# Performance work log

Measured on AMD Instinct MI355X. Metric: run time of the kernel, lower is better.

Reference implementation:

```python
import jax, jax.numpy as jnp
import numpy as np

B, S, E, H = 4, 2048, 1024, 16
D = E // H  # head_dim = 64

def setup_inputs() -> dict:
    key = jax.random.key(0)
    ks = jax.random.split(key, 9)
    std = 1.0 / np.sqrt(E)
    return {
        "x":  jax.random.normal(ks[0], (B, S, E), jnp.float32),
        "Wq": jax.random.uniform(ks[1], (E, E), jnp.float32, -std, std),
        "bq": jax.random.uniform(ks[2], (E,),   jnp.float32, -std, std),
        "Wk": jax.random.uniform(ks[3], (E, E), jnp.float32, -std, std),
        "bk": jax.random.uniform(ks[4], (E,),   jnp.float32, -std, std),
        "Wv": jax.random.uniform(ks[5], (E, E), jnp.float32, -std, std),
        "bv": jax.random.uniform(ks[6], (E,),   jnp.float32, -std, std),
        "Wo": jax.random.uniform(ks[7], (E, E), jnp.float32, -std, std),
        "bo": jax.random.uniform(ks[8], (E,),   jnp.float32, -std, std),
    }

def reference(x, Wq, bq, Wk, bk, Wv, bv, Wo, bo):
    b, s, e = x.shape
    # QKV projections (weights stored as [in,out] == torch W.T applied as x @ W)
    q = (x @ Wq + bq).reshape(b, s, H, D).transpose(0, 2, 1, 3)  # [B,H,S,D]
    k = (x @ Wk + bk).reshape(b, s, H, D).transpose(0, 2, 1, 3)
    v = (x @ Wv + bv).reshape(b, s, H, D).transpose(0, 2, 1, 3)
    scores = jnp.einsum('bhqd,bhkd->bhqk', q, k) / jnp.sqrt(jnp.float32(D))
    causal = jnp.triu(jnp.ones((s, s), bool), k=1)  # True above diagonal
    scores = jnp.where(causal, -jnp.inf, scores)
    p = jax.nn.softmax(scores, axis=-1)  # dropout disabled (eval mode)
    out = jnp.einsum('bhqk,bhkd->bhqd', p, v)  # [B,H,S,D]
    out = out.transpose(0, 2, 1, 3).reshape(b, s, e)
    return out @ Wo + bo
```

## Files before the change

kernel.cpp:

```cpp
#include <hip/hip_runtime.h>
#include <math.h>

#define E_DIM 1024
#define B_DIM 4
#define S_DIM 2048
#define H_DIM 16
#define D_HEAD 64
#define M_DIM (B_DIM * S_DIM)
#define LOG2E 1.44269504f

typedef _Float16 half8 __attribute__((ext_vector_type(8)));
typedef _Float16 half4 __attribute__((ext_vector_type(4)));
typedef __fp16  fp16x2 __attribute__((ext_vector_type(2)));
typedef float floatx4 __attribute__((ext_vector_type(4)));
typedef unsigned uint2v __attribute__((ext_vector_type(2)));
#define MFMA_F16(a, b, c) __builtin_amdgcn_mfma_f32_16x16x32_f16(a, b, c, 0, 0, 0)

#if __has_builtin(__builtin_amdgcn_exp2f)
#define EXP2F(x) __builtin_amdgcn_exp2f(x)
#else
#define EXP2F(x) exp2f(x)
#endif

union H4 { fp16x2 h2[2]; half4 h4; };
union H8 { fp16x2 h2[4]; half8 h8; };

#define GLDS16(g, l)                                                          \
    __builtin_amdgcn_global_load_lds(                                         \
        (const __attribute__((address_space(1))) void*)(g),                   \
        (__attribute__((address_space(3))) void*)(l), 16, 0, 0)

__device__ const int SEG_QBLK[40] = {3,4,5,6,7,7,8,8,9,9,10,10,11,11,11,12,12,12,
                                     13,13,13,14,14,14,15,15,15,15,
                                     2,6,10,14, 1,5,9,13, 0,4,8,12};
__device__ const int SEG_SEG[40]  = {0,0,0,0,0,1,0,1,0,1,0,1,0,1,2,0,1,2,
                                     0,1,2,0,1,2,0,1,2,3,
                                     0,1,2,3, 0,1,2,3, 0,1,2,3};
__device__ const int SEG_BASE[16] = {0,1,2,3,4,6,8,10,12,15,18,21,24,28,32,36};

__global__ __launch_bounds__(256) void cvt_x(
    const float* __restrict__ X, _Float16* __restrict__ Xh)
{
    size_t i = ((size_t)blockIdx.x * 256 + threadIdx.x) * 8;
    float4 a = *(const float4*)&X[i];
    float4 b = *(const float4*)&X[i + 4];
    half8 h = {(_Float16)a.x, (_Float16)a.y, (_Float16)a.z, (_Float16)a.w,
               (_Float16)b.x, (_Float16)b.y, (_Float16)b.z, (_Float16)b.w};
    *(half8*)&Xh[i] = h;
}

__global__ __launch_bounds__(256) void cvt_w(
    const float* __restrict__ W0, const float* __restrict__ W1,
    const float* __restrict__ W2, const float* __restrict__ W3,
    _Float16* __restrict__ T0, _Float16* __restrict__ T1,
    _Float16* __restrict__ T2, _Float16* __restrict__ T3)
{
    const int z = blockIdx.z;
    const float* W = (z == 0) ? W0 : (z == 1) ? W1 : (z == 2) ? W2 : W3;
    _Float16*   T  = (z == 0) ? T0 : (z == 1) ? T1 : (z == 2) ? T2 : T3;
    const int k0 = blockIdx.x * 64, n0 = blockIdx.y * 64;
    const int tid = threadIdx.x;
    __shared__ float t[64][65];
#pragma unroll
    for (int it = 0; it < 4; it++) {
        int r = it * 16 + (tid >> 4);
        int c = (tid & 15) * 4;
        float4 v = *(const float4*)&W[(size_t)(k0 + r) * E_DIM + n0 + c];
        t[r][c] = v.x; t[r][c + 1] = v.y; t[r][c + 2] = v.z; t[r][c + 3] = v.w;
    }
    __syncthreads();
#pragma unroll
    for (int it = 0; it < 2; it++) {
        int n = it * 32 + (tid >> 3);
        int kk = (tid & 7) * 8;
        half8 h;
#pragma unroll
        for (int j = 0; j < 8; j++) h[j] = (_Float16)t[kk + j][n];
        *(half8*)&T[(size_t)(n0 + n) * E_DIM + k0 + kk] = h;
    }
}

#define STAGE128(t, s)                                                        \
    _Pragma("unroll") for (int i = 0; i < 4; i++) {                           \
        GLDS16(aS[i] + (t) * 64, As + (s) * 8192 + dOff[i]);                  \
        GLDS16(bS[i] + (t) * 64, Bs + (s) * 8192 + dOff[i]);                  \
    }

#define PH128_READ_A(mh)                                                      \
    _Pragma("unroll") for (int am = 0; am < 2; am++)                          \
        _Pragma("unroll") for (int kh = 0; kh < 2; kh++)                      \
            a_[am][kh] = *(const half8*)&As[sb +                              \
                (wr * 64 + ((mh) * 2 + am) * 16 + m16) * 64 +                 \
                (((kh * 4 + quad) ^ sw8) * 8)];

#define PH128_READ_B(nh)                                                      \
    _Pragma("unroll") for (int bn = 0; bn < 2; bn++)                          \
        _Pragma("unroll") for (int kh = 0; kh < 2; kh++)                      \
            b_[bn][kh] = *(const half8*)&Bs[sb +                              \
                (wc * 64 + ((nh) * 2 + bn) * 16 + m16) * 64 +                 \
                (((kh * 4 + quad) ^ sw8) * 8)];

#define PH128_MFMA(mh, nh)                                                    \
    __builtin_amdgcn_s_setprio(1);                                            \
    _Pragma("unroll") for (int am = 0; am < 2; am++)                          \
        _Pragma("unroll") for (int bn = 0; bn < 2; bn++)                      \
            acc[(mh) * 2 + am][(nh) * 2 + bn] =                               \
                MFMA_F16(a_[am][1], b_[bn][1],                                \
                    MFMA_F16(a_[am][0], b_[bn][0],                            \
                             acc[(mh) * 2 + am][(nh) * 2 + bn]));             \
    __builtin_amdgcn_s_setprio(0);

#define GEMM128_CORE(Aptr, Bptr)                                              \
    const int tid = threadIdx.x;                                              \
    const int wave = tid >> 6, lane = tid & 63;                               \
    const int m16 = lane & 15, quad = lane >> 4;                              \
    const int wr = wave >> 1, wc = wave & 1;                                  \
    const int m0 = blockIdx.x * 128, n0 = blockIdx.y * 128;                   \
    const int sw8 = m16 & 7;                                                  \
    __shared__ _Float16 As[2 * 8192];                                         \
    __shared__ _Float16 Bs[2 * 8192];                                         \
    floatx4 acc[4][4];                                                        \
    const floatx4 zf = {0.f, 0.f, 0.f, 0.f};                                  \
    _Pragma("unroll") for (int i = 0; i < 4; i++)                             \
        _Pragma("unroll") for (int j = 0; j < 4; j++) acc[i][j] = zf;         \
    const _Float16* aS[4];                                                    \
    const _Float16* bS[4];                                                    \
    int dOff[4];                                                              \
    _Pragma("unroll") for (int i = 0; i < 4; i++) {                           \
        int u = i * 256 + tid;                                                \
        int ru = u >> 3, cb = (u & 7) ^ (ru & 7);                             \
        aS[i] = (Aptr) + (size_t)(m0 + ru) * E_DIM + cb * 8;                  \
        bS[i] = (Bptr) + (size_t)(n0 + ru) * E_DIM + cb * 8;                  \
        dOff[i] = i * 2048 + wave * 512;                                      \
    }                                                                         \
    STAGE128(0, 0);                                                           \
    STAGE128(1, 1);                                                           \
    asm volatile("s_waitcnt vmcnt(8)" ::: "memory");                          \
    __builtin_amdgcn_s_barrier();                                             \
    half8 a_[2][2], b_[2][2];                                                 \
    for (int t = 0; t < 16; t++) {                                            \
        const int sb = (t & 1) * 8192;                                        \
        PH128_READ_A(0); PH128_READ_B(0); PH128_MFMA(0, 0);                   \
        PH128_READ_B(1); PH128_MFMA(0, 1);                                    \
        PH128_READ_A(1); PH128_MFMA(1, 1);                                    \
        PH128_READ_B(0); PH128_MFMA(1, 0);                                    \
        if (t + 1 < 16) {                                                     \
            asm volatile("s_waitcnt lgkmcnt(0)" ::: "memory");                \
            __builtin_amdgcn_s_barrier();                                     \
            if (t + 2 < 16) {                                                 \
                STAGE128(t + 2, t & 1);                                       \
                asm volatile("s_waitcnt vmcnt(8)" ::: "memory");              \
            } else {                                                          \
                asm volatile("s_waitcnt vmcnt(0)" ::: "memory");              \
            }                                                                 \
            __builtin_amdgcn_s_barrier();                                     \
        }                                                                     \
    }

__global__ __launch_bounds__(256) void qkv_mfma(
    const _Float16* __restrict__ Xh,
    const _Float16* __restrict__ Tq, const float* __restrict__ bq,
    const _Float16* __restrict__ Tk, const float* __restrict__ bk,
    const _Float16* __restrict__ Tv, const float* __restrict__ bv,
    _Float16* __restrict__ Qo, _Float16* __restrict__ Ko, _Float16* __restrict__ Vo)
{
    const int z = blockIdx.z;
    const _Float16* Wt   = (z == 0) ? Tq : (z == 1) ? Tk : Tv;
    const float*    bias = (z == 0) ? bq : (z == 1) ? bk : bv;

    GEMM128_CORE(Xh, Wt)

    if (z == 2) {
#pragma unroll
        for (int nt = 0; nt < 4; nt++) {
            int n = n0 + wc * 64 + nt * 16 + m16;
            int h = n >> 6, d = n & 63;
            int dt = d >> 4, ld = d & 15;
            float bias_v = bias[n];
#pragma unroll
            for (int mt = 0; mt < 4; mt++) {
                int m_b = m0 + wr * 64 + mt * 16 + quad * 4;
                int b = m_b >> 11, s = m_b & 2047;
                int bh = b * H_DIM + h;
                int c = s >> 6, kl = s & 63;
                int kh = kl >> 5, q8 = (kl >> 2) & 3, j0 = ((kl >> 4) & 1) * 4;
                size_t off = ((size_t)bh * 32 + c) * 4096
                           + (size_t)(((dt * 2 + kh) * 64 + q8 * 16 + ld) * 8 + j0);
                half4 hv;
#pragma unroll
                for (int r = 0; r < 4; r++) hv[r] = (_Float16)(acc[mt][nt][r] + bias_v);
                *(half4*)&Vo[off] = hv;
            }
        }
    } else {
        _Float16* Out = (z == 0) ? Qo : Ko;
        const float sc = (z == 0) ? 0.125f * LOG2E : 1.0f;
#pragma unroll
        for (int nt = 0; nt < 4; nt++) {
            int n = n0 + wc * 64 + nt * 16 + m16;
            int h = n >> 6, d = n & 63;
            int dh = d >> 5, qd = (d >> 3) & 3, j = d & 7;
            float bias_v = bias[n];
#pragma unroll
            for (int mt = 0; mt < 4; mt++) {
#pragma unroll
                for (int r = 0; r < 4; r++) {
                    int m = m0 + wr * 64 + mt * 16 + quad * 4 + r;
                    int b = m >> 11, s = m & 2047;
                    int bh = b * H_DIM + h;
                    size_t off;
                    if (z == 0) {
                        int qblk = s >> 7, qq = s & 127;
                        int sub = qq >> 4, lq = qq & 15;
                        off = ((size_t)bh * 16 + qblk) * 8192
                            + (size_t)(((sub * 2 + dh) * 64 + qd * 16 + lq) * 8 + j);
                    } else {
                        int c = s >> 6, kl = s & 63;
                        int kt = kl >> 4, lk = kl & 15;
                        off = ((size_t)bh * 32 + c) * 4096
                            + (size_t)(((kt * 2 + dh) * 64 + qd * 16 + lk) * 8 + j);
                    }
                    Out[off] = (_Float16)((acc[mt][nt][r] + bias_v) * sc);
                }
            }
        }
    }
}

__global__ __launch_bounds__(256) void out_mfma(
    const _Float16* __restrict__ Oh, const _Float16* __restrict__ To,
    const float* __restrict__ bias, float* __restrict__ Out)
{
    GEMM128_CORE(Oh, To)

#pragma unroll
    for (int nt = 0; nt < 4; nt++) {
        int n = n0 + wc * 64 + nt * 16 + m16;
        float bias_v = bias[n];
#pragma unroll
        for (int mt = 0; mt < 4; mt++) {
#pragma unroll
            for (int r = 0; r < 4; r++) {
                int m = m0 + wr * 64 + mt * 16 + quad * 4 + r;
                Out[(size_t)m * E_DIM + n] = acc[mt][nt][r] + bias_v;
            }
        }
    }
}

__global__ __launch_bounds__(256) void attn_mfma(
    const _Float16* __restrict__ Qb, const _Float16* __restrict__ Kb,
    const _Float16* __restrict__ Vb, _Float16* __restrict__ Opart,
    float* __restrict__ Mv, float* __restrict__ Lv, _Float16* __restrict__ O)
{
    const int L = blockIdx.x;
    const int xcd = L & 7;
    const int u = L >> 3;
    const int bh = xcd * 8 + (u / 40);
    const int wid = u % 40;
    const int wave = threadIdx.x >> 6;
    const int qblk = SEG_QBLK[wid];
    const int seg  = SEG_SEG[wid];
    const int q0 = qblk * 128;
    const int c0 = seg * 8;
    const int c1 = min(c0 + 8, 2 * qblk + 2);
    const bool solo = (c0 == 0) && (c1 == 2 * qblk + 2);
    const int lane = threadIdx.x & 63;
    const int m16 = lane & 15, quad = lane >> 4;

    const int qmin = q0 + wave * 32;
    const int qmax = qmin + 31;
    const int c1w = min(c1, (qmax >> 6) + 1);

    const _Float16* gQ = Qb + ((size_t)bh * 16 + qblk) * 8192 + wave * 2048 + lane * 8;
    half8 qf[2][2];
#pragma unroll
    for (int mt = 0; mt < 2; mt++)
#pragma unroll
        for (int dh = 0; dh < 2; dh++)
            qf[mt][dh] = *(const half8*)&gQ[(mt * 2 + dh) * 512];

    const floatx4 zf  = {0.f, 0.f, 0.f, 0.f};
    const floatx4 cm4 = {-4.f, -4.f, -4.f, -4.f};
    half8 onev;
#pragma unroll
    for (int j = 0; j < 8; j++) onev[j] = (_Float16)1.0f;

    floatx4 acco[2][4];
    floatx4 lacc[2];
#pragma unroll
    for (int mt = 0; mt < 2; mt++) {
        lacc[mt] = zf;
#pragma unroll
        for (int dt = 0; dt < 4; dt++) acco[mt][dt] = zf;
    }

    const _Float16* gK = Kb + ((size_t)bh * 32 + c0) * 4096 + lane * 8;
    const _Float16* gV = Vb + ((size_t)bh * 32 + c0) * 4096 + lane * 8;

    half8 kf[4][2];
#pragma unroll
    for (int kt = 0; kt < 4; kt++)
#pragma unroll
        for (int dh = 0; dh < 2; dh++)
            kf[kt][dh] = *(const half8*)&gK[(kt * 2 + dh) * 512];
    gK += 4096;

    for (int c = c0; c < c1w; c++) {
        const int k0 = c * 64;

        half8 vf[4][2];
#pragma unroll
        for (int dt = 0; dt < 4; dt++)
#pragma unroll
            for (int kh = 0; kh < 2; kh++)
                vf[dt][kh] = *(const half8*)&gV[(dt * 2 + kh) * 512];
        gV += 4096;

        floatx4 sf[2][4];
        __builtin_amdgcn_s_setprio(1);
#pragma unroll
        for (int kt = 0; kt < 4; kt++)
#pragma unroll
            for (int mt = 0; mt < 2; mt++)
                sf[mt][kt] = MFMA_F16(kf[kt][1], qf[mt][1],
                               MFMA_F16(kf[kt][0], qf[mt][0], cm4));
        __builtin_amdgcn_s_setprio(0);

        if (c + 1 < c1w) {
#pragma unroll
            for (int kt = 0; kt < 4; kt++)
#pragma unroll
                for (int dh = 0; dh < 2; dh++)
                    kf[kt][dh] = *(const half8*)&gK[(kt * 2 + dh) * 512];
            gK += 4096;
        }

        const bool full = (k0 + 63 <= qmin);
#pragma unroll
        for (int mt = 0; mt < 2; mt++) {
            const int qg = qmin + mt * 16 + m16;
#pragma unroll
            for (int kt = 0; kt < 4; kt++)
#pragma unroll
                for (int r = 0; r < 4; r++) {
                    if (!full) {
                        int key = k0 + kt * 16 + quad * 4 + r;
                        if (key > qg) sf[mt][kt][r] = -INFINITY;
                    }
                }

            H8 u8[2];
#pragma unroll
            for (int kt = 0; kt < 4; kt++) {
                float e0 = EXP2F(sf[mt][kt][0]);
                float e1 = EXP2F(sf[mt][kt][1]);
                float e2 = EXP2F(sf[mt][kt][2]);
                float e3 = EXP2F(sf[mt][kt][3]);
                u8[kt >> 1].h2[(kt & 1) * 2]     = __builtin_amdgcn_cvt_pkrtz(e0, e1);
                u8[kt >> 1].h2[(kt & 1) * 2 + 1] = __builtin_amdgcn_cvt_pkrtz(e2, e3);
            }

            __builtin_amdgcn_s_setprio(1);
            lacc[mt] = MFMA_F16(onev, u8[1].h8,
                         MFMA_F16(onev, u8[0].h8, lacc[mt]));
#pragma unroll
            for (int dt = 0; dt < 4; dt++)
                acco[mt][dt] = MFMA_F16(vf[dt][1], u8[1].h8,
                                 MFMA_F16(vf[dt][0], u8[0].h8, acco[mt][dt]));
            __builtin_amdgcn_s_setprio(0);
        }
    }

    if (solo) {
        const int b = bh >> 4;
        const int h = bh & (H_DIM - 1);
#pragma unroll
        for (int mt = 0; mt < 2; mt++) {
            float inv = 1.f / lacc[mt][0];
            int q = qmin + mt * 16 + m16;
            _Float16* dst = O + (size_t)(b * S_DIM + q) * E_DIM + h * 64;
#pragma unroll
            for (int dt = 0; dt < 4; dt++) {
                H4 u4;
                u4.h2[0] = __builtin_amdgcn_cvt_pkrtz(acco[mt][dt][0] * inv, acco[mt][dt][1] * inv);
                u4.h2[1] = __builtin_amdgcn_cvt_pkrtz(acco[mt][dt][2] * inv, acco[mt][dt][3] * inv);
                *(half4*)&dst[dt * 16 + quad * 4] = u4.h4;
            }
        }
    } else {
        const size_t prow = ((size_t)bh * 40 + SEG_BASE[qblk] + seg) * 128;
#pragma unroll
        for (int mt = 0; mt < 2; mt++) {
            int lq = wave * 32 + mt * 16 + m16;
            if (quad == 0) {
                Lv[prow + lq] = lacc[mt][0];
            }
            _Float16* dst = Opart + (prow + lq) * 64;
#pragma unroll
            for (int dt = 0; dt < 4; dt++) {
                H4 u4;
                u4.h2[0] = __builtin_amdgcn_cvt_pkrtz(acco[mt][dt][0], acco[mt][dt][1]);
                u4.h2[1] = __builtin_amdgcn_cvt_pkrtz(acco[mt][dt][2], acco[mt][dt][3]);
                *(half4*)&dst[dt * 16 + quad * 4] = u4.h4;
            }
        }
    }
}

__global__ __launch_bounds__(256) void attn_combine(
    const _Float16* __restrict__ Opart, const float* __restrict__ Mv,
    const float* __restrict__ Lv, _Float16* __restrict__ O)
{
    const int qb = blockIdx.x + 4, bh = blockIdx.y;
    const int nseg = (qb >> 2) + 1;
    const size_t pbase = ((size_t)bh * 40 + SEG_BASE[qb]) * 128;
    const int t = threadIdx.x;
    const int r = t >> 1, dh = (t & 1) * 32;

    float L = 0.f;
    for (int s = 0; s < nseg; s++) L += Lv[pbase + s * 128 + r];
    const float invL = 1.f / L;

    const int b = bh >> 4, h = bh & (H_DIM - 1);
    const int q = qb * 128 + r;
    _Float16* dst = O + (size_t)(b * S_DIM + q) * E_DIM + h * 64 + dh;
#pragma unroll
    for (int d0 = 0; d0 < 32; d0 += 8) {
        float acc[8] = {0.f, 0.f, 0.f, 0.f, 0.f, 0.f, 0.f, 0.f};
        for (int s = 0; s < nseg; s++) {
            half8 v = *(const half8*)&Opart[(pbase + s * 128 + r) * 64 + dh + d0];
#pragma unroll
            for (int j = 0; j < 8; j++) acc[j] += (float)v[j];
        }
        half8 o;
#pragma unroll
        for (int j = 0; j < 8; j++) o[j] = (_Float16)(acc[j] * invL);
        *(half8*)&dst[d0] = o;
    }
}

extern "C" void kernel_launch(void* const* d_in, const int* in_sizes, int n_in,
                              void* d_out, int out_size, void* d_ws, size_t ws_size,
                              hipStream_t stream) {
    const float* x  = (const float*)d_in[0];
    const float* Wq = (const float*)d_in[1];
    const float* bq = (const float*)d_in[2];
    const float* Wk = (const float*)d_in[3];
    const float* bk = (const float*)d_in[4];
    const float* Wv = (const float*)d_in[5];
    const float* bv = (const float*)d_in[6];
    const float* Wo = (const float*)d_in[7];
    const float* bo = (const float*)d_in[8];

    const size_t SZ = (size_t)M_DIM * E_DIM;
    const size_t WZ = (size_t)E_DIM * E_DIM;
    _Float16* Xh = (_Float16*)d_ws;
    _Float16* Tq = Xh + SZ;
    _Float16* Tk = Tq + WZ;
    _Float16* Tv = Tk + WZ;
    _Float16* To = Tv + WZ;
    _Float16* Qb = To + WZ;
    _Float16* Kb = Qb + SZ;
    _Float16* Vb = Kb + SZ;
    _Float16* Opart = Vb + SZ;
    float* Mv = (float*)(Opart + (size_t)2560 * 8192);
    float* Lv = Mv + 2560 * 128;
    _Float16* Oh = Xh;

    cvt_x<<<dim3(M_DIM * E_DIM / 2048), 256, 0, stream>>>(x, Xh);
    cvt_w<<<dim3(16, 16, 4), 256, 0, stream>>>(Wq, Wk, Wv, Wo, Tq, Tk, Tv, To);

    qkv_mfma<<<dim3(M_DIM / 128, E_DIM / 128, 3), 256, 0, stream>>>(
        Xh, Tq, bq, Tk, bk, Tv, bv, Qb, Kb, Vb);

    attn_mfma<<<dim3(8 * 8 * 40), 256, 0, stream>>>(
        Qb, Kb, Vb, Opart, Mv, Lv, Oh);

    attn_combine<<<dim3(12, B_DIM * H_DIM), 256, 0, stream>>>(Opart, Mv, Lv, Oh);

    out_mfma<<<dim3(M_DIM / 128, E_DIM / 128), 256, 0, stream>>>(
        Oh, To, bo, (float*)d_out);
}
```

Before: 282.1 us.

## Replace split-KV attention and combine kernel with paired causal query blocks

Attention work is now split across 512 blocks instead of 2560 split-KV segment blocks. Each block handles two query blocks (pair and 15-pair) of one head in sequence, so every block carries a similar causal workload. This removes the partial-output and row-sum writes to workspace and the separate attn_combine launch, and each block normalizes and writes the final output directly. In exchange the grid is much smaller (about two blocks per CU), so there are fewer resident waves to hide the latency of K/V loads, which come straight from global memory.

```diff
diff --git a/kernel.cpp b/kernel.cpp
--- a/kernel.cpp
+++ b/kernel.cpp
@@ -29,14 +29,6 @@
     __builtin_amdgcn_global_load_lds(                                         \
         (const __attribute__((address_space(1))) void*)(g),                   \
         (__attribute__((address_space(3))) void*)(l), 16, 0, 0)
-
-__device__ const int SEG_QBLK[40] = {3,4,5,6,7,7,8,8,9,9,10,10,11,11,11,12,12,12,
-                                     13,13,13,14,14,14,15,15,15,15,
-                                     2,6,10,14, 1,5,9,13, 0,4,8,12};
-__device__ const int SEG_SEG[40]  = {0,0,0,0,0,1,0,1,0,1,0,1,0,1,2,0,1,2,
-                                     0,1,2,0,1,2,0,1,2,3,
-                                     0,1,2,3, 0,1,2,3, 0,1,2,3};
-__device__ const int SEG_BASE[16] = {0,1,2,3,4,6,8,10,12,15,18,21,24,28,32,36};
 
 __global__ __launch_bounds__(256) void cvt_x(
     const float* __restrict__ X, _Float16* __restrict__ Xh)
@@ -250,35 +242,16 @@
 
 __global__ __launch_bounds__(256) void attn_mfma(
     const _Float16* __restrict__ Qb, const _Float16* __restrict__ Kb,
-    const _Float16* __restrict__ Vb, _Float16* __restrict__ Opart,
-    float* __restrict__ Mv, float* __restrict__ Lv, _Float16* __restrict__ O)
+    const _Float16* __restrict__ Vb, _Float16* __restrict__ O)
 {
     const int L = blockIdx.x;
     const int xcd = L & 7;
     const int u = L >> 3;
-    const int bh = xcd * 8 + (u / 40);
-    const int wid = u % 40;
+    const int bh = xcd * 8 + (u >> 3);
+    const int pair = u & 7;
     const int wave = threadIdx.x >> 6;
-    const int qblk = SEG_QBLK[wid];
-    const int seg  = SEG_SEG[wid];
-    const int q0 = qblk * 128;
-    const int c0 = seg * 8;
-    const int c1 = min(c0 + 8, 2 * qblk + 2);
-    const bool solo = (c0 == 0) && (c1 == 2 * qblk + 2);
     const int lane = threadIdx.x & 63;
     const int m16 = lane & 15, quad = lane >> 4;
-
-    const int qmin = q0 + wave * 32;
-    const int qmax = qmin + 31;
-    const int c1w = min(c1, (qmax >> 6) + 1);
-
-    const _Float16* gQ = Qb + ((size_t)bh * 16 + qblk) * 8192 + wave * 2048 + lane * 8;
-    half8 qf[2][2];
-#pragma unroll
-    for (int mt = 0; mt < 2; mt++)
-#pragma unroll
-        for (int dh = 0; dh < 2; dh++)
-            qf[mt][dh] = *(const half8*)&gQ[(mt * 2 + dh) * 512];
 
     const floatx4 zf  = {0.f, 0.f, 0.f, 0.f};
     const floatx4 cm4 = {-4.f, -4.f, -4.f, -4.f};
@@ -286,100 +259,114 @@
 #pragma unroll
     for (int j = 0; j < 8; j++) onev[j] = (_Float16)1.0f;
 
-    floatx4 acco[2][4];
-    floatx4 lacc[2];
-#pragma unroll
-    for (int mt = 0; mt < 2; mt++) {
-        lacc[mt] = zf;
-#pragma unroll
-        for (int dt = 0; dt < 4; dt++) acco[mt][dt] = zf;
-    }
-
-    const _Float16* gK = Kb + ((size_t)bh * 32 + c0) * 4096 + lane * 8;
-    const _Float16* gV = Vb + ((size_t)bh * 32 + c0) * 4096 + lane * 8;
-
-    half8 kf[4][2];
-#pragma unroll
-    for (int kt = 0; kt < 4; kt++)
-#pragma unroll
-        for (int dh = 0; dh < 2; dh++)
-            kf[kt][dh] = *(const half8*)&gK[(kt * 2 + dh) * 512];
-    gK += 4096;
-
-    for (int c = c0; c < c1w; c++) {
-        const int k0 = c * 64;
-
-        half8 vf[4][2];
-#pragma unroll
-        for (int dt = 0; dt < 4; dt++)
-#pragma unroll
-            for (int kh = 0; kh < 2; kh++)
-                vf[dt][kh] = *(const half8*)&gV[(dt * 2 + kh) * 512];
-        gV += 4096;
-
-        floatx4 sf[2][4];
-        __builtin_amdgcn_s_setprio(1);
+    const int b_ = bh >> 4;
+    const int h_ = bh & (H_DIM - 1);
+
+    for (int half = 0; half < 2; half++) {
+        const int qblk = half ? (15 - pair) : pair;
+        const int qmin = qblk * 128 + wave * 32;
+        const int c1w = ((qmin + 31) >> 6) + 1;
+
+        const _Float16* gQ = Qb + ((size_t)bh * 16 + qblk) * 8192
+                                + wave * 2048 + lane * 8;
+        half8 qf[2][2];
+#pragma unroll
+        for (int mt = 0; mt < 2; mt++)
+#pragma unroll
+            for (int dh = 0; dh < 2; dh++)
+                qf[mt][dh] = *(const half8*)&gQ[(mt * 2 + dh) * 512];
+
+        floatx4 acco[2][4];
+        floatx4 lacc[2];
+#pragma unroll
+        for (int mt = 0; mt < 2; mt++) {
+            lacc[mt] = zf;
+#pragma unroll
+            for (int dt = 0; dt < 4; dt++) acco[mt][dt] = zf;
+        }
+
+        const _Float16* gK = Kb + (size_t)bh * 131072 + lane * 8;
+        const _Float16* gV = Vb + (size_t)bh * 131072 + lane * 8;
+
+        half8 kf[4][2];
 #pragma unroll
         for (int kt = 0; kt < 4; kt++)
 #pragma unroll
-            for (int mt = 0; mt < 2; mt++)
-                sf[mt][kt] = MFMA_F16(kf[kt][1], qf[mt][1],
-                               MFMA_F16(kf[kt][0], qf[mt][0], cm4));
-        __builtin_amdgcn_s_setprio(0);
-
-        if (c + 1 < c1w) {
+            for (int dh = 0; dh < 2; dh++)
+                kf[kt][dh] = *(const half8*)&gK[(kt * 2 + dh) * 512];
+        gK += 4096;
+
+        for (int c = 0; c < c1w; c++) {
+            const int k0 = c * 64;
+
+            half8 vf[4][2];
+#pragma unroll
+            for (int dt = 0; dt < 4; dt++)
+#pragma unroll
+                for (int kh = 0; kh < 2; kh++)
+                    vf[dt][kh] = *(const half8*)&gV[(dt * 2 + kh) * 512];
+            gV += 4096;
+
+            floatx4 sf[2][4];
+            __builtin_amdgcn_s_setprio(1);
 #pragma unroll
             for (int kt = 0; kt < 4; kt++)
 #pragma unroll
-                for (int dh = 0; dh < 2; dh++)
-                    kf[kt][dh] = *(const half8*)&gK[(kt * 2 + dh) * 512];
-            gK += 4096;
-        }
-
-        const bool full = (k0 + 63 <= qmin);
-#pragma unroll
-        for (int mt = 0; mt < 2; mt++) {
-            const int qg = qmin + mt * 16 + m16;
-#pragma unroll
-            for (int kt = 0; kt < 4; kt++)
-#pragma unroll
-                for (int r = 0; r < 4; r++) {
-                    if (!full) {
-                        int key = k0 + kt * 16 + quad * 4 + r;
-                        if (key > qg) sf[mt][kt][r] = -INFINITY;
+                for (int mt = 0; mt < 2; mt++)
+                    sf[mt][kt] = MFMA_F16(kf[kt][1], qf[mt][1],
+                                   MFMA_F16(kf[kt][0], qf[mt][0], cm4));
+            __builtin_amdgcn_s_setprio(0);
+
+            if (c + 1 < c1w) {
+#pragma unroll
+                for (int kt = 0; kt < 4; kt++)
+#pragma unroll
+                    for (int dh = 0; dh < 2; dh++)
+                        kf[kt][dh] = *(const half8*)&gK[(kt * 2 + dh) * 512];
+                gK += 4096;
+            }
+
+            const bool full = (k0 + 63 <= qmin);
+#pragma unroll
+            for (int mt = 0; mt < 2; mt++) {
+                const int qg = qmin + mt * 16 + m16;
+#pragma unroll
+                for (int kt = 0; kt < 4; kt++)
+#pragma unroll
+                    for (int r = 0; r < 4; r++) {
+                        if (!full) {
+                            int key = k0 + kt * 16 + quad * 4 + r;
+                            if (key > qg) sf[mt][kt][r] = -INFINITY;
+                        }
                     }
+
+                H8 u8[2];
+#pragma unroll
+                for (int kt = 0; kt < 4; kt++) {
+                    float e0 = EXP2F(sf[mt][kt][0]);
+                    float e1 = EXP2F(sf[mt][kt][1]);
+                    float e2 = EXP2F(sf[mt][kt][2]);
+                    float e3 = EXP2F(sf[mt][kt][3]);
+                    u8[kt >> 1].h2[(kt & 1) * 2]     = __builtin_amdgcn_cvt_pkrtz(e0, e1);
+                    u8[kt >> 1].h2[(kt & 1) * 2 + 1] = __builtin_amdgcn_cvt_pkrtz(e2, e3);
                 }
 
-            H8 u8[2];
-#pragma unroll
-            for (int kt = 0; kt < 4; kt++) {
-                float e0 = EXP2F(sf[mt][kt][0]);
-                float e1 = EXP2F(sf[mt][kt][1]);
-                float e2 = EXP2F(sf[mt][kt][2]);
-                float e3 = EXP2F(sf[mt][kt][3]);
-                u8[kt >> 1].h2[(kt & 1) * 2]     = __builtin_amdgcn_cvt_pkrtz(e0, e1);
-                u8[kt >> 1].h2[(kt & 1) * 2 + 1] = __builtin_amdgcn_cvt_pkrtz(e2, e3);
-            }
-
-            __builtin_amdgcn_s_setprio(1);
-            lacc[mt] = MFMA_F16(onev, u8[1].h8,
-                         MFMA_F16(onev, u8[0].h8, lacc[mt]));
-#pragma unroll
-            for (int dt = 0; dt < 4; dt++)
-                acco[mt][dt] = MFMA_F16(vf[dt][1], u8[1].h8,
-                                 MFMA_F16(vf[dt][0], u8[0].h8, acco[mt][dt]));
-            __builtin_amdgcn_s_setprio(0);
-        }
-    }
-
-    if (solo) {
-        const int b = bh >> 4;
-        const int h = bh & (H_DIM - 1);
+                __builtin_amdgcn_s_setprio(1);
+                lacc[mt] = MFMA_F16(onev, u8[1].h8,
+                             MFMA_F16(onev, u8[0].h8, lacc[mt]));
+#pragma unroll
+                for (int dt = 0; dt < 4; dt++)
+                    acco[mt][dt] = MFMA_F16(vf[dt][1], u8[1].h8,
+                                     MFMA_F16(vf[dt][0], u8[0].h8, acco[mt][dt]));
+                __builtin_amdgcn_s_setprio(0);
+            }
+        }
+
 #pragma unroll
         for (int mt = 0; mt < 2; mt++) {
             float inv = 1.f / lacc[mt][0];
             int q = qmin + mt * 16 + m16;
-            _Float16* dst = O + (size_t)(b * S_DIM + q) * E_DIM + h * 64;
+            _Float16* dst = O + (size_t)(b_ * S_DIM + q) * E_DIM + h_ * 64;
 #pragma unroll
             for (int dt = 0; dt < 4; dt++) {
                 H4 u4;
@@ -388,55 +375,6 @@
                 *(half4*)&dst[dt * 16 + quad * 4] = u4.h4;
             }
         }
-    } else {
-        const size_t prow = ((size_t)bh * 40 + SEG_BASE[qblk] + seg) * 128;
-#pragma unroll
-        for (int mt = 0; mt < 2; mt++) {
-            int lq = wave * 32 + mt * 16 + m16;
-            if (quad == 0) {
-                Lv[prow + lq] = lacc[mt][0];
-            }
-            _Float16* dst = Opart + (prow + lq) * 64;
-#pragma unroll
-            for (int dt = 0; dt < 4; dt++) {
-                H4 u4;
-                u4.h2[0] = __builtin_amdgcn_cvt_pkrtz(acco[mt][dt][0], acco[mt][dt][1]);
-                u4.h2[1] = __builtin_amdgcn_cvt_pkrtz(acco[mt][dt][2], acco[mt][dt][3]);
-                *(half4*)&dst[dt * 16 + quad * 4] = u4.h4;
-            }
-        }
-    }
-}
-
-__global__ __launch_bounds__(256) void attn_combine(
-    const _Float16* __restrict__ Opart, const float* __restrict__ Mv,
-    const float* __restrict__ Lv, _Float16* __restrict__ O)
-{
-    const int qb = blockIdx.x + 4, bh = blockIdx.y;
-    const int nseg = (qb >> 2) + 1;
-    const size_t pbase = ((size_t)bh * 40 + SEG_BASE[qb]) * 128;
-    const int t = threadIdx.x;
-    const int r = t >> 1, dh = (t & 1) * 32;
-
-    float L = 0.f;
-    for (int s = 0; s < nseg; s++) L += Lv[pbase + s * 128 + r];
-    const float invL = 1.f / L;
-
-    const int b = bh >> 4, h = bh & (H_DIM - 1);
-    const int q = qb * 128 + r;
-    _Float16* dst = O + (size_t)(b * S_DIM + q) * E_DIM + h * 64 + dh;
-#pragma unroll
-    for (int d0 = 0; d0 < 32; d0 += 8) {
-        float acc[8] = {0.f, 0.f, 0.f, 0.f, 0.f, 0.f, 0.f, 0.f};
-        for (int s = 0; s < nseg; s++) {
-            half8 v = *(const half8*)&Opart[(pbase + s * 128 + r) * 64 + dh + d0];
-#pragma unroll
-            for (int j = 0; j < 8; j++) acc[j] += (float)v[j];
-        }
-        half8 o;
-#pragma unroll
-        for (int j = 0; j < 8; j++) o[j] = (_Float16)(acc[j] * invL);
-        *(half8*)&dst[d0] = o;
     }
 }
 
@@ -463,9 +401,6 @@
     _Float16* Qb = To + WZ;
     _Float16* Kb = Qb + SZ;
     _Float16* Vb = Kb + SZ;
-    _Float16* Opart = Vb + SZ;
-    float* Mv = (float*)(Opart + (size_t)2560 * 8192);
-    float* Lv = Mv + 2560 * 128;
     _Float16* Oh = Xh;
 
     cvt_x<<<dim3(M_DIM * E_DIM / 2048), 256, 0, stream>>>(x, Xh);
@@ -474,10 +409,7 @@
     qkv_mfma<<<dim3(M_DIM / 128, E_DIM / 128, 3), 256, 0, stream>>>(
         Xh, Tq, bq, Tk, bk, Tv, bv, Qb, Kb, Vb);
 
-    attn_mfma<<<dim3(8 * 8 * 40), 256, 0, stream>>>(
-        Qb, Kb, Vb, Opart, Mv, Lv, Oh);
-
-    attn_combine<<<dim3(12, B_DIM * H_DIM), 256, 0, stream>>>(Opart, Mv, Lv, Oh);
+    attn_mfma<<<dim3(512), 256, 0, stream>>>(Qb, Kb, Vb, Oh);
 
     out_mfma<<<dim3(M_DIM / 128, E_DIM / 128), 256, 0, stream>>>(
         Oh, To, bo, (float*)d_out);
```

After: 275.9 us. -2.2%, faster.
